# Optimization experiments

Hardware: AMD Instinct MI355X
Metric: run time of the kernel (lower is better)

## Reference

```python
import jax, jax.numpy as jnp
import numpy as np

DIM = 1024
NUM_HEADS = 16
DIM_HEAD = 64
INNER = NUM_HEADS * DIM_HEAD  # 1024
B, N = 2, 2048


def setup_inputs() -> dict:
    key = jax.random.key(0)
    k1, k2, k3 = jax.random.split(key, 3)
    x = jax.random.normal(k1, (B, N, DIM), dtype=jnp.float32)
    # nn.Linear(dim, inner*3, bias=False): weight [3*inner, dim]; y = x @ W^T
    w_qkv = jax.random.normal(k2, (3 * INNER, DIM), dtype=jnp.float32) * (DIM ** -0.5)
    # to_out: Linear(inner, dim) with bias
    w_out = jax.random.normal(k3, (DIM, INNER), dtype=jnp.float32) * (INNER ** -0.5)
    b_out = jnp.zeros((DIM,), dtype=jnp.float32)
    return {"x": x, "w_qkv": w_qkv, "w_out": w_out, "b_out": b_out}


def reference(x, w_qkv, w_out, b_out):
    b, n, d = x.shape
    scale = DIM_HEAD ** -0.5
    qkv = jnp.einsum('bnd,ed->bne', x, w_qkv)  # [b, n, 3*inner]
    q, k, v = jnp.split(qkv, 3, axis=-1)
    # [b, n, h, dh] -> [b, h, n, dh]
    reshape = lambda t: t.reshape(b, n, NUM_HEADS, DIM_HEAD).transpose(0, 2, 1, 3)
    q, k, v = reshape(q), reshape(k), reshape(v)
    dots = jnp.einsum('bhqd,bhkd->bhqk', q, k) * scale  # [b, h, n, n]
    attn = jax.nn.softmax(dots, axis=-1)
    out = jnp.einsum('bhqk,bhkd->bhqd', attn, v)
    out = out.transpose(0, 2, 1, 3).reshape(b, n, INNER)
    out = jnp.einsum('bni,oi->bno', out, w_out) + b_out
    return out
```

## Files before the change

kernel.cpp:

```cpp
#include <hip/hip_runtime.h>
#include <hip/hip_bf16.h>
#include <stdint.h>

typedef unsigned short u16;
typedef short bf16x8 __attribute__((ext_vector_type(8)));
typedef float f32x4 __attribute__((ext_vector_type(4)));
typedef float f32x16 __attribute__((ext_vector_type(16)));
typedef u16 u16x4 __attribute__((ext_vector_type(4)));
typedef unsigned int uint2v __attribute__((ext_vector_type(2)));

#define DIMX  1024
#define NHEAD 16
#define DH    64
#define INNER 1024
#define BATCH 2
#define SEQ   2048
#define MTOT  (BATCH*SEQ)
#define EQKV  (3*INNER)

__device__ __forceinline__ u16 f2bf(float f) {
  unsigned int x = __float_as_uint(f);
  unsigned int r = (x + 0x7FFFu + ((x >> 16) & 1u)) >> 16;
  return (u16)r;
}

__device__ __forceinline__ unsigned int cvtpk(float lo, float hi) {
  unsigned int r;
  asm("v_cvt_pk_bf16_f32 %0, %1, %2" : "=v"(r) : "v"(lo), "v"(hi));
  return r;
}

__device__ __forceinline__ void plswap_u(unsigned int& x, unsigned int& y) {
  auto r = __builtin_amdgcn_permlane32_swap(x, y, false, false);
  x = r[0]; y = r[1];
}
__device__ __forceinline__ void plswap_f2(float v, float& a, float& b) {
  unsigned int x = __float_as_uint(v), y = __float_as_uint(v);
  auto r = __builtin_amdgcn_permlane32_swap(x, y, false, false);
  a = __uint_as_float(r[0]); b = __uint_as_float(r[1]);
}

__device__ __forceinline__ void async16(void* lds, const void* g) {
  __builtin_amdgcn_global_load_lds(
      (const __attribute__((address_space(1))) unsigned int*)g,
      (__attribute__((address_space(3))) unsigned int*)lds,
      16, 0, 0);
}

__device__ __forceinline__ int swz4(int r) { return (r ^ (r >> 2)) & 3; }

__global__ void cvt_kernel(const float* __restrict__ in, u16* __restrict__ out, int n4) {
  int i = blockIdx.x * blockDim.x + threadIdx.x;
  if (i < n4) {
    float4 v = ((const float4*)in)[i];
    u16x4 o;
    o[0] = f2bf(v.x); o[1] = f2bf(v.y); o[2] = f2bf(v.z); o[3] = f2bf(v.w);
    ((u16x4*)out)[i] = o;
  }
}

__global__ __launch_bounds__(256) void gemm_qkv(const u16* __restrict__ X, const u16* __restrict__ W,
                                                u16* __restrict__ Qo, u16* __restrict__ Ko,
                                                u16* __restrict__ Vt) {
  __shared__ short sAll[16384];
  short* sA = sAll;
  short* sB = sAll + 8192;
  const int tid = threadIdx.x;
  const int wv = tid >> 6, l = tid & 63;
  const int lo = l & 15, hi = l >> 4;
  const int wr = wv >> 1, wc = wv & 1;

  int lin = blockIdx.x;
  int wgid = (lin & 7) * 96 + (lin >> 3);
  const int bx = wgid / 32;
  const int by = wgid % 32;
  const int tn = bx * 128, tm = by * 128;

  f32x4 acc[4][4];
#pragma unroll
  for (int i = 0; i < 4; i++)
#pragma unroll
    for (int j = 0; j < 4; j++) acc[i][j] = (f32x4){0.f, 0.f, 0.f, 0.f};

  auto stage = [&](int buf, int kt) {
    int k0 = kt * 32;
    int off = buf * 4096;
#pragma unroll
    for (int c = 0; c < 2; c++) {
      int R0 = wv * 32 + c * 16;
      int r = R0 + (l >> 2);
      int sc = ((l & 3) ^ swz4(r)) * 8;
      async16(&sA[off + R0 * 32], &X[(size_t)(tm + r) * DIMX + k0 + sc]);
      async16(&sB[off + R0 * 32], &W[(size_t)(tn + r) * DIMX + k0 + sc]);
    }
  };

  stage(0, 0);
  __syncthreads();

  for (int kt = 0; kt < DIMX / 32; kt++) {
    const int buf = kt & 1;
    if (kt + 1 < DIMX / 32) stage(buf ^ 1, kt + 1);
    bf16x8 af[4], bf[4];
#pragma unroll
    for (int i = 0; i < 4; i++) {
      int r = wr * 64 + i * 16 + lo;
      af[i] = *(const bf16x8*)&sA[buf * 4096 + r * 32 + ((hi ^ swz4(r)) * 8)];
    }
#pragma unroll
    for (int j = 0; j < 4; j++) {
      int r = wc * 64 + j * 16 + lo;
      bf[j] = *(const bf16x8*)&sB[buf * 4096 + r * 32 + ((hi ^ swz4(r)) * 8)];
    }
#pragma unroll
    for (int i = 0; i < 4; i++)
#pragma unroll
      for (int j = 0; j < 4; j++)
        acc[i][j] = __builtin_amdgcn_mfma_f32_16x16x32_bf16(af[i], bf[j], acc[i][j], 0, 0, 0);
    __syncthreads();
  }

  const int cls = tn >> 10;
  const float scale = 0.125f * 1.44269504088896f;

  if (cls < 2) {
#pragma unroll
    for (int i = 0; i < 4; i++) {
      int mbase = tm + wr * 64 + i * 16 + hi * 4;
#pragma unroll
      for (int j = 0; j < 4; j++) {
        int e = tn + wc * 64 + j * 16 + lo;
        int e2 = e & 1023, h = e2 >> 6, d = e2 & 63;
#pragma unroll
        for (int r = 0; r < 4; r++) {
          int mm = mbase + r;
          int b = mm >> 11, n = mm & 2047;
          float v = acc[i][j][r];
          if (cls == 0)
            Qo[(((size_t)(b * NHEAD + h)) * SEQ + n) * DH + d] = f2bf(v * scale);
          else
            Ko[(((size_t)(b * NHEAD + h)) * SEQ + n) * DH + d] = f2bf(v);
        }
      }
    }
  } else {
#pragma unroll
    for (int i = 0; i < 4; i++) {
#pragma unroll
      for (int j = 0; j < 4; j++) {
        int e = wc * 64 + j * 16 + lo;
#pragma unroll
        for (int r = 0; r < 4; r++) {
          int n = wr * 64 + i * 16 + hi * 4 + r;
          sAll[e * 128 + (((n >> 3) ^ (e & 15)) * 8) + (n & 7)] = (short)f2bf(acc[i][j][r]);
        }
      }
    }
    __syncthreads();
    int er = tid >> 1, half = tid & 1;
    int e2 = tn + er - 2048;
    int h = e2 >> 6, d = e2 & 63;
    int b = tm >> 11, nb = tm & 2047;
    u16* dst = &Vt[(((size_t)(b * NHEAD + h)) * DH + d) * SEQ + nb + half * 64];
#pragma unroll
    for (int k = 0; k < 8; k++) {
      int phys = (half * 8 + k) ^ (er & 15);
      bf16x8 v = *(const bf16x8*)&sAll[er * 128 + phys * 8];
      *(bf16x8*)&dst[k * 8] = v;
    }
  }
}

__global__ __launch_bounds__(256) void attn_kernel(const u16* __restrict__ Q, const u16* __restrict__ Kd,
                                                   const u16* __restrict__ Vt, u16* __restrict__ O) {
  __shared__ short sK[2][64 * 64];
  __shared__ short sV[2][64 * 64];
  const int tid = threadIdx.x, wv = tid >> 6, l = tid & 63;
  const int l31 = l & 31, hi5 = l >> 5, l7 = l & 7;

  int lin = blockIdx.y * gridDim.x + blockIdx.x;
  int wgid = (lin & 7) * 64 + (lin >> 3);
  int bx = wgid & 15;
  int bh = wgid >> 4;

  const int qw = bx * 128 + wv * 32;
  const u16* Qb = Q + (size_t)bh * SEQ * DH;
  const u16* Kb = Kd + (size_t)bh * SEQ * DH;
  const u16* Vb = Vt + (size_t)bh * DH * SEQ;

  bf16x8 qf[4];
#pragma unroll
  for (int kd = 0; kd < 4; kd++)
    qf[kd] = *(const bf16x8*)&Qb[(size_t)(qw + l31) * DH + kd * 16 + hi5 * 8];

  f32x16 o0, o1;
#pragma unroll
  for (int r = 0; r < 16; r++) { o0[r] = 0.f; o1[r] = 0.f; }
  float mrun = -1e30f, lsum = 0.f;
  const float THR = 11.0f;

  auto stage = [&](int buf, int t) {
    int kv0 = t * 64;
#pragma unroll
    for (int c = 0; c < 2; c++) {
      int rbase = wv * 16 + c * 8;
      int gr = rbase + (l >> 3);
      int sc = ((l & 7) ^ (l >> 3)) * 8;
      async16(&sK[buf][rbase * 64], &Kb[(size_t)(kv0 + gr) * DH + sc]);
      async16(&sV[buf][rbase * 64], &Vb[(size_t)gr * SEQ + kv0 + sc]);
    }
  };

  stage(0, 0);
  __syncthreads();

  for (int t = 0; t < SEQ / 64; t++) {
    const int cur = t & 1;
    if (t + 1 < SEQ / 64) stage(cur ^ 1, t + 1);

    f32x16 s0, s1;
#pragma unroll
    for (int r = 0; r < 16; r++) { s0[r] = 0.f; s1[r] = 0.f; }
#pragma unroll
    for (int kd = 0; kd < 4; kd++) {
      int c16 = ((kd * 2 + hi5) ^ l7) * 8;
      bf16x8 k0 = *(const bf16x8*)&sK[cur][l31 * 64 + c16];
      bf16x8 k1 = *(const bf16x8*)&sK[cur][(32 + l31) * 64 + c16];
      s0 = __builtin_amdgcn_mfma_f32_32x32x16_bf16(k0, qf[kd], s0, 0, 0, 0);
      s1 = __builtin_amdgcn_mfma_f32_32x32x16_bf16(k1, qf[kd], s1, 0, 0, 0);
    }

    float tr[16];
#pragma unroll
    for (int r = 0; r < 16; r++) tr[r] = fmaxf(s0[r], s1[r]);
#pragma unroll
    for (int st = 8; st > 0; st >>= 1)
#pragma unroll
      for (int r = 0; r < st; r++) tr[r] = fmaxf(tr[r], tr[r + st]);
    float mxa, mxb;
    plswap_f2(tr[0], mxa, mxb);
    float mx = fmaxf(mxa, mxb);

    if (!__all(mx <= mrun + THR)) {
      float mnew = fmaxf(mrun, mx);
      float alpha = __builtin_amdgcn_exp2f(mrun - mnew);
      mrun = mnew;
      lsum *= alpha;
      o0 *= alpha;
      o1 *= alpha;
    }

    float sm[16];
#pragma unroll
    for (int r = 0; r < 16; r++) {
      s0[r] = __builtin_amdgcn_exp2f(s0[r] - mrun);
      s1[r] = __builtin_amdgcn_exp2f(s1[r] - mrun);
      sm[r] = s0[r] + s1[r];
    }
#pragma unroll
    for (int st = 8; st > 0; st >>= 1)
#pragma unroll
      for (int r = 0; r < st; r++) sm[r] += sm[r + st];
    lsum += sm[0];

    bf16x8 pa[4];
#pragma unroll
    for (int ks = 0; ks < 4; ks++) {
      const int sft = (ks & 1) * 8;
      float e0 = (ks < 2) ? s0[sft + 0] : s1[sft + 0];
      float e1 = (ks < 2) ? s0[sft + 1] : s1[sft + 1];
      float e2 = (ks < 2) ? s0[sft + 2] : s1[sft + 2];
      float e3 = (ks < 2) ? s0[sft + 3] : s1[sft + 3];
      float e4 = (ks < 2) ? s0[sft + 4] : s1[sft + 4];
      float e5 = (ks < 2) ? s0[sft + 5] : s1[sft + 5];
      float e6 = (ks < 2) ? s0[sft + 6] : s1[sft + 6];
      float e7 = (ks < 2) ? s0[sft + 7] : s1[sft + 7];
      unsigned int w0 = cvtpk(e0, e1);
      unsigned int w1 = cvtpk(e2, e3);
      unsigned int w2 = cvtpk(e4, e5);
      unsigned int w3 = cvtpk(e6, e7);
      plswap_u(w0, w2);
      plswap_u(w1, w3);
      union { unsigned int w[4]; bf16x8 v; } u;
      u.w[0] = w0; u.w[1] = w1; u.w[2] = w2; u.w[3] = w3;
      pa[ks] = u.v;
    }

#pragma unroll
    for (int ks = 0; ks < 4; ks++) {
      int c16 = ((ks * 2 + hi5) ^ l7) * 8;
      bf16x8 v0 = *(const bf16x8*)&sV[cur][l31 * 64 + c16];
      bf16x8 v1 = *(const bf16x8*)&sV[cur][(32 + l31) * 64 + c16];
      o0 = __builtin_amdgcn_mfma_f32_32x32x16_bf16(v0, pa[ks], o0, 0, 0, 0);
      o1 = __builtin_amdgcn_mfma_f32_32x32x16_bf16(v1, pa[ks], o1, 0, 0, 0);
    }
    __syncthreads();
  }

  float la, lb;
  plswap_f2(lsum, la, lb);
  float inv = 1.0f / (la + lb);

  int b = bh >> 4, h = bh & 15;
  int q = qw + l31;
  size_t orow = ((size_t)(b * SEQ + q)) * INNER + h * 64;
#pragma unroll
  for (int half = 0; half < 2; half++) {
    const f32x16& oo = half ? o1 : o0;
#pragma unroll
    for (int g = 0; g < 4; g++) {
      uint2v pk2;
      pk2[0] = cvtpk(oo[g * 4 + 0] * inv, oo[g * 4 + 1] * inv);
      pk2[1] = cvtpk(oo[g * 4 + 2] * inv, oo[g * 4 + 3] * inv);
      int dv = half * 32 + g * 8 + 4 * hi5;
      *(uint2v*)&O[orow + dv] = pk2;
    }
  }
}

__global__ __launch_bounds__(256) void gemm_out(const u16* __restrict__ A, const u16* __restrict__ W,
                                                const float* __restrict__ bias, float* __restrict__ out) {
  __shared__ short sAll[16384];
  short* sA = sAll;
  short* sB = sAll + 8192;
  const int tid = threadIdx.x;
  const int wv = tid >> 6, l = tid & 63;
  const int lo = l & 15, hi = l >> 4;
  const int wr = wv >> 1, wc = wv & 1;

  int lin = blockIdx.x;
  int wgid = (lin & 7) * 32 + (lin >> 3);
  const int bx = wgid / 32;
  const int by = wgid % 32;
  const int tn = bx * 128, tm = by * 128;

  f32x4 acc[4][4];
#pragma unroll
  for (int i = 0; i < 4; i++)
#pragma unroll
    for (int j = 0; j < 4; j++) acc[i][j] = (f32x4){0.f, 0.f, 0.f, 0.f};

  auto stage = [&](int buf, int kt) {
    int k0 = kt * 32;
    int off = buf * 4096;
#pragma unroll
    for (int c = 0; c < 2; c++) {
      int R0 = wv * 32 + c * 16;
      int r = R0 + (l >> 2);
      int sc = ((l & 3) ^ swz4(r)) * 8;
      async16(&sA[off + R0 * 32], &A[(size_t)(tm + r) * INNER + k0 + sc]);
      async16(&sB[off + R0 * 32], &W[(size_t)(tn + r) * INNER + k0 + sc]);
    }
  };

  stage(0, 0);
  __syncthreads();

  for (int kt = 0; kt < INNER / 32; kt++) {
    const int buf = kt & 1;
    if (kt + 1 < INNER / 32) stage(buf ^ 1, kt + 1);
    bf16x8 af[4], bf[4];
#pragma unroll
    for (int i = 0; i < 4; i++) {
      int r = wr * 64 + i * 16 + lo;
      af[i] = *(const bf16x8*)&sA[buf * 4096 + r * 32 + ((hi ^ swz4(r)) * 8)];
    }
#pragma unroll
    for (int j = 0; j < 4; j++) {
      int r = wc * 64 + j * 16 + lo;
      bf[j] = *(const bf16x8*)&sB[buf * 4096 + r * 32 + ((hi ^ swz4(r)) * 8)];
    }
#pragma unroll
    for (int i = 0; i < 4; i++)
#pragma unroll
      for (int j = 0; j < 4; j++)
        acc[i][j] = __builtin_amdgcn_mfma_f32_16x16x32_bf16(af[i], bf[j], acc[i][j], 0, 0, 0);
    __syncthreads();
  }

#pragma unroll
  for (int i = 0; i < 4; i++) {
    int mbase = tm + wr * 64 + i * 16 + hi * 4;
#pragma unroll
    for (int j = 0; j < 4; j++) {
      int col = tn + wc * 64 + j * 16 + lo;
      float bv = bias[col];
#pragma unroll
      for (int r = 0; r < 4; r++)
        out[(size_t)(mbase + r) * DIMX + col] = acc[i][j][r] + bv;
    }
  }
}

extern "C" void kernel_launch(void* const* d_in, const int* in_sizes, int n_in,
                              void* d_out, int out_size, void* d_ws, size_t ws_size,
                              hipStream_t stream) {
  const float* x     = (const float*)d_in[0];
  const float* w_qkv = (const float*)d_in[1];
  const float* w_out = (const float*)d_in[2];
  const float* b_out = (const float*)d_in[3];

  char* ws = (char*)d_ws;
  u16* xb    = (u16*)(ws);
  u16* wqkvb = (u16*)(ws + (size_t)8  * (1<<20));
  u16* woutb = (u16*)(ws + (size_t)14 * (1<<20));
  u16* Qd    = (u16*)(ws + (size_t)16 * (1<<20));
  u16* Kdd   = (u16*)(ws + (size_t)24 * (1<<20));
  u16* Vtd   = (u16*)(ws + (size_t)32 * (1<<20));
  u16* Od    = (u16*)(ws + (size_t)40 * (1<<20));

  cvt_kernel<<<(MTOT * DIMX / 4 + 255) / 256, 256, 0, stream>>>(x, xb, MTOT * DIMX / 4);
  cvt_kernel<<<(EQKV * DIMX / 4 + 255) / 256, 256, 0, stream>>>(w_qkv, wqkvb, EQKV * DIMX / 4);
  cvt_kernel<<<(DIMX * INNER / 4 + 255) / 256, 256, 0, stream>>>(w_out, woutb, DIMX * INNER / 4);

  gemm_qkv<<<768, 256, 0, stream>>>(xb, wqkvb, Qd, Kdd, Vtd);
  attn_kernel<<<dim3(SEQ / 128, BATCH * NHEAD), 256, 0, stream>>>(Qd, Kdd, Vtd, Od);
  gemm_out<<<256, 256, 0, stream>>>(Od, woutb, b_out, (float*)d_out);
}
```

Baseline: 133.2 us.

## Load K/V fragments directly from global memory instead of LDS staging

Removes the double-buffered shared-memory staging of K and V tiles in the attention kernel. Each wave now loads its MFMA operand fragments straight from global memory (relying on L1/L2 caching) and drops the per-iteration barrier. This avoids LDS traffic and synchronisation, but each of the 4 waves redundantly fetches the same K/V tile, and there is no async prefetch to hide global latency.

```diff
diff --git a/kernel.cpp b/kernel.cpp
--- a/kernel.cpp
+++ b/kernel.cpp
@@ -173,10 +173,8 @@
 
 __global__ __launch_bounds__(256) void attn_kernel(const u16* __restrict__ Q, const u16* __restrict__ Kd,
                                                    const u16* __restrict__ Vt, u16* __restrict__ O) {
-  __shared__ short sK[2][64 * 64];
-  __shared__ short sV[2][64 * 64];
   const int tid = threadIdx.x, wv = tid >> 6, l = tid & 63;
-  const int l31 = l & 31, hi5 = l >> 5, l7 = l & 7;
+  const int l31 = l & 31, hi5 = l >> 5;
 
   int lin = blockIdx.y * gridDim.x + blockIdx.x;
   int wgid = (lin & 7) * 64 + (lin >> 3);
@@ -199,35 +197,33 @@
   float mrun = -1e30f, lsum = 0.f;
   const float THR = 11.0f;
 
-  auto stage = [&](int buf, int t) {
-    int kv0 = t * 64;
-#pragma unroll
-    for (int c = 0; c < 2; c++) {
-      int rbase = wv * 16 + c * 8;
-      int gr = rbase + (l >> 3);
-      int sc = ((l & 7) ^ (l >> 3)) * 8;
-      async16(&sK[buf][rbase * 64], &Kb[(size_t)(kv0 + gr) * DH + sc]);
-      async16(&sV[buf][rbase * 64], &Vb[(size_t)gr * SEQ + kv0 + sc]);
-    }
-  };
-
-  stage(0, 0);
-  __syncthreads();
+  const u16* Krow0 = &Kb[(size_t)l31 * DH + hi5 * 8];
+  const u16* Krow1 = &Kb[(size_t)(32 + l31) * DH + hi5 * 8];
+  const u16* Vrow0 = &Vb[(size_t)l31 * SEQ + hi5 * 8];
+  const u16* Vrow1 = &Vb[(size_t)(32 + l31) * SEQ + hi5 * 8];
 
   for (int t = 0; t < SEQ / 64; t++) {
-    const int cur = t & 1;
-    if (t + 1 < SEQ / 64) stage(cur ^ 1, t + 1);
+    const int kv0 = t * 64;
+
+    bf16x8 kf0[4], kf1[4], vf0[4], vf1[4];
+#pragma unroll
+    for (int kd = 0; kd < 4; kd++) {
+      kf0[kd] = *(const bf16x8*)&Krow0[(size_t)kv0 * DH + kd * 16];
+      kf1[kd] = *(const bf16x8*)&Krow1[(size_t)kv0 * DH + kd * 16];
+    }
+#pragma unroll
+    for (int ks = 0; ks < 4; ks++) {
+      vf0[ks] = *(const bf16x8*)&Vrow0[kv0 + ks * 16];
+      vf1[ks] = *(const bf16x8*)&Vrow1[kv0 + ks * 16];
+    }
 
     f32x16 s0, s1;
 #pragma unroll
     for (int r = 0; r < 16; r++) { s0[r] = 0.f; s1[r] = 0.f; }
 #pragma unroll
     for (int kd = 0; kd < 4; kd++) {
-      int c16 = ((kd * 2 + hi5) ^ l7) * 8;
-      bf16x8 k0 = *(const bf16x8*)&sK[cur][l31 * 64 + c16];
-      bf16x8 k1 = *(const bf16x8*)&sK[cur][(32 + l31) * 64 + c16];
-      s0 = __builtin_amdgcn_mfma_f32_32x32x16_bf16(k0, qf[kd], s0, 0, 0, 0);
-      s1 = __builtin_amdgcn_mfma_f32_32x32x16_bf16(k1, qf[kd], s1, 0, 0, 0);
+      s0 = __builtin_amdgcn_mfma_f32_32x32x16_bf16(kf0[kd], qf[kd], s0, 0, 0, 0);
+      s1 = __builtin_amdgcn_mfma_f32_32x32x16_bf16(kf1[kd], qf[kd], s1, 0, 0, 0);
     }
 
     float tr[16];
@@ -288,13 +284,9 @@
 
 #pragma unroll
     for (int ks = 0; ks < 4; ks++) {
-      int c16 = ((ks * 2 + hi5) ^ l7) * 8;
-      bf16x8 v0 = *(const bf16x8*)&sV[cur][l31 * 64 + c16];
-      bf16x8 v1 = *(const bf16x8*)&sV[cur][(32 + l31) * 64 + c16];
-      o0 = __builtin_amdgcn_mfma_f32_32x32x16_bf16(v0, pa[ks], o0, 0, 0, 0);
-      o1 = __builtin_amdgcn_mfma_f32_32x32x16_bf16(v1, pa[ks], o1, 0, 0, 0);
-    }
-    __syncthreads();
+      o0 = __builtin_amdgcn_mfma_f32_32x32x16_bf16(vf0[ks], pa[ks], o0, 0, 0, 0);
+      o1 = __builtin_amdgcn_mfma_f32_32x32x16_bf16(vf1[ks], pa[ks], o1, 0, 0, 0);
+    }
   }
 
   float la, lb;
```

Result: slower. 196.2 us (+47.4%).
